# Performance work log

Hardware: AMD Instinct MI355X
Metric: run time of the kernel (lower is better)

The kernel has to match this reference:

```python
import jax, jax.numpy as jnp
import numpy as np
import math

N_HEADS = 8
INPUT_DIM = 128
EMBED_DIM = 128
KEY_DIM = 16
VAL_DIM = 16
BATCH = 2
SEQ = 4096


def setup_inputs() -> dict:
    key = jax.random.key(0)
    kq, kh, km, k1, k2, k3, k4 = jax.random.split(key, 7)
    q = jax.random.normal(kq, (BATCH, SEQ, INPUT_DIM), dtype=jnp.float32)
    h = jax.random.normal(kh, (BATCH, SEQ, INPUT_DIM), dtype=jnp.float32)
    mask = jax.random.randint(km, (BATCH, SEQ, SEQ), 0, 2).astype(jnp.bool_)
    # uniform(-stdv, stdv) with stdv = 1/sqrt(last_dim), matching init_parameters()
    def uni(k, shape):
        stdv = 1.0 / math.sqrt(shape[-1])
        return jax.random.uniform(k, shape, jnp.float32, -stdv, stdv)
    W_query = uni(k1, (N_HEADS, INPUT_DIM, KEY_DIM))
    W_key = uni(k2, (N_HEADS, INPUT_DIM, KEY_DIM))
    W_val = uni(k3, (N_HEADS, INPUT_DIM, VAL_DIM))
    W_out = uni(k4, (N_HEADS, VAL_DIM, EMBED_DIM))
    return {"q": q, "h": h, "mask": mask, "W_query": W_query,
            "W_key": W_key, "W_val": W_val, "W_out": W_out}


def reference(q, h, mask, W_query, W_key, W_val, W_out):
    norm = 1.0 / math.sqrt(KEY_DIM)
    # per-head projections: (h,b,n,k)
    Q = jnp.einsum('bni,hik->hbnk', q, W_query)
    K = jnp.einsum('bmi,hik->hbmk', h, W_key)
    V = jnp.einsum('bmi,hiv->hbmv', h, W_val)
    # full dense score tensor (h,b,n,m) — matches original materialization
    compat = norm * jnp.einsum('hbnk,hbmk->hbnm', Q, K)
    m = mask[None]  # broadcast over heads
    compat = jnp.where(m, -jnp.inf, compat)
    attn = jax.nn.softmax(compat, axis=-1)
    attn = jnp.where(m, 0.0, attn)
    heads = jnp.einsum('hbnm,hbmv->hbnv', attn, V)
    out = jnp.einsum('hbnv,hve->bne', heads, W_out)
    return out
```

## Files before the change

### kernel.cpp

```cpp
#include <hip/hip_runtime.h>
#include <stdint.h>

#define SEQ 4096
#define DIM 128
#define NHEADS 8
#define HDK 16

typedef __bf16 bf16x2 __attribute__((ext_vector_type(2)));
typedef __bf16 bf16x8 __attribute__((ext_vector_type(8)));
typedef float f32x16 __attribute__((ext_vector_type(16)));
typedef float f32x4 __attribute__((ext_vector_type(4)));
typedef unsigned uint2v __attribute__((ext_vector_type(2)));
typedef unsigned uint4v __attribute__((ext_vector_type(4)));

__device__ inline unsigned short f2bf(float x) {
  unsigned u = __builtin_bit_cast(unsigned, x);
  u = (u + 0x7FFFu + ((u >> 16) & 1u)) >> 16;
  return (unsigned short)u;
}
__device__ inline unsigned pkbf(float lo, float hi) {
  return (unsigned)f2bf(lo) | ((unsigned)f2bf(hi) << 16);
}
__device__ inline unsigned pkbf_fast(float lo, float hi) {
  bf16x2 t;
  t[0] = (__bf16)lo;
  t[1] = (__bf16)hi;
  return __builtin_bit_cast(unsigned, t);
}
__device__ inline float fexp2(float x) {
#if __has_builtin(__builtin_amdgcn_exp2f)
  return __builtin_amdgcn_exp2f(x);
#else
  return exp2f(x);
#endif
}
__device__ inline float keep_and(float e, unsigned mrsi, int kvc) {
#if __has_builtin(__builtin_amdgcn_sbfe)
  const unsigned m = (unsigned)__builtin_amdgcn_sbfe((int)mrsi, kvc, 1);
#else
  const unsigned m = (unsigned)(((int)(mrsi << (31 - kvc))) >> 31);
#endif
  return __builtin_bit_cast(float, __builtin_bit_cast(unsigned, e) & m);
}

__global__ __launch_bounds__(256) void k_pre(
    const float* __restrict__ qin, const float* __restrict__ hin,
    const float* __restrict__ Wq, const float* __restrict__ Wk,
    const float* __restrict__ Wv, const void* __restrict__ maskp,
    unsigned short* __restrict__ Qp, unsigned short* __restrict__ Kp,
    unsigned short* __restrict__ Vt32, unsigned* __restrict__ bits) {
  __shared__ float Wl[128][128];
  __shared__ float inl[8][128];
  const int bid = (int)blockIdx.x;
  const int tid = threadIdx.x;

  if (bid >= 896) {
    unsigned* Vt32w = (unsigned*)Vt32;
    const int base = (bid - 896) * 256 + tid;
    #pragma unroll
    for (int j = 0; j < 32; ++j) {
      const int w = base + j * 1024;
      const int bh = w >> 11, n2 = w & 2047;
      Vt32w[((size_t)bh * 32 + 16) * 2048 + n2] = 0x3F803F80u;
    }
    return;
  }

  if (bid >= 384) {
    unsigned (*mlds)[17] = (unsigned (*)[17])Wl;
    const unsigned*      mw = (const unsigned*)maskp;
    const unsigned char* m8 = (const unsigned char*)maskp;
    bool wordmode = true;
    #pragma unroll
    for (int i = 0; i < 32; ++i) {
      unsigned w = mw[i];
      if (!(w == 0u || w == 1u || w == 0x3F800000u)) wordmode = false;
    }
    const int mb = bid - 384;
    const int b = mb >> 8;
    const int rowbase = (mb & 255) * 16;
    const int kt = tid & 127;
    #pragma unroll
    for (int p = 0; p < 8; ++p) {
      const int rl = p * 2 + (tid >> 7);
      const size_t g = ((size_t)b * SEQ + rowbase + rl) * SEQ + kt * 32;
      unsigned word = 0;
      if (wordmode) {
        uint4v w0 = *(const uint4v*)(mw + g);
        uint4v w1 = *(const uint4v*)(mw + g + 4);
        uint4v w2 = *(const uint4v*)(mw + g + 8);
        uint4v w3 = *(const uint4v*)(mw + g + 12);
        uint4v w4 = *(const uint4v*)(mw + g + 16);
        uint4v w5 = *(const uint4v*)(mw + g + 20);
        uint4v w6 = *(const uint4v*)(mw + g + 24);
        uint4v w7 = *(const uint4v*)(mw + g + 28);
        const uint4v wv[8] = { w0, w1, w2, w3, w4, w5, w6, w7 };
        #pragma unroll
        for (int j = 0; j < 8; ++j)
          #pragma unroll
          for (int e = 0; e < 4; ++e) {
            const unsigned w = wv[j][e];
            word |= ((w | (0u - w)) >> 31) << (4 * j + e);
          }
      } else {
        uint4v c0 = *(const uint4v*)(m8 + g);
        uint4v c1 = *(const uint4v*)(m8 + g + 16);
        const uint4v cv[2] = { c0, c1 };
        #pragma unroll
        for (int j = 0; j < 2; ++j)
          #pragma unroll
          for (int e = 0; e < 4; ++e) {
            unsigned w = cv[j][e];
            #pragma unroll
            for (int by = 0; by < 4; ++by) {
              word |= ((w & 0xFFu) ? 1u : 0u) << (16 * j + 4 * e + by);
              w >>= 8;
            }
          }
      }
      mlds[kt][rl] = word;
    }
    __syncthreads();
    #pragma unroll
    for (int j = 0; j < 8; ++j) {
      const int idx = tid + 256 * j;
      const int k2 = idx >> 4, rl = idx & 15;
      bits[((size_t)b * 128 + k2) * SEQ + rowbase + rl] = mlds[k2][rl];
    }
    return;
  }

  const int mat = bid >> 7;
  const int xb  = bid & 127;
  const float* in = (mat == 0) ? qin : hin;
  const float* W  = (mat == 0) ? Wq : (mat == 1 ? Wk : Wv);
  for (int e = tid; e < 128 * 128; e += 256) {
    int i = e >> 7, c = e & 127;
    Wl[i][c] = W[((size_t)((c >> 4) * 128 + i)) * 16 + (c & 15)];
  }
  const int r  = tid >> 5;
  const int cg = (tid & 31) << 2;
  const size_t rb = (size_t)xb * 64;
  const float SCALE_Q = 0.25f * 1.4426950408889634f;
  for (int pass = 0; pass < 8; ++pass) {
    __syncthreads();
    size_t row0 = rb + pass * 8;
    for (int e = tid; e < 8 * 128; e += 256)
      inl[e >> 7][e & 127] = in[(row0 + (e >> 7)) * 128 + (e & 127)];
    __syncthreads();
    f32x4 acc = {0.f, 0.f, 0.f, 0.f};
    #pragma unroll 8
    for (int i = 0; i < 128; ++i) {
      float a = inl[r][i];
      acc += a * *(const f32x4*)&Wl[i][cg];
    }
    size_t grow = row0 + r;
    if (mat == 0) {
      uint2v o = { pkbf(acc[0] * SCALE_Q, acc[1] * SCALE_Q),
                   pkbf(acc[2] * SCALE_Q, acc[3] * SCALE_Q) };
      *(uint2v*)(Qp + grow * DIM + cg) = o;
    } else if (mat == 1) {
      uint2v o = { pkbf(acc[0], acc[1]), pkbf(acc[2], acc[3]) };
      *(uint2v*)(Kp + grow * DIM + cg) = o;
    } else {
      size_t b = grow >> 12, n = grow & 4095;
      #pragma unroll
      for (int j = 0; j < 4; ++j) {
        const int c = cg + j;
        Vt32[((size_t)(b * 8 + (c >> 4)) * 32 + (c & 15)) * SEQ + n] =
            f2bf(acc[j]);
      }
    }
  }
}

__global__ __launch_bounds__(512, 4) void k_flash(
    const unsigned short* __restrict__ Qp, const unsigned short* __restrict__ Kp,
    const unsigned short* __restrict__ Vt32, const unsigned* __restrict__ bits,
    float* __restrict__ parts, float* __restrict__ Lb, int NT) {
  const int tid  = threadIdx.x;
  const int wv   = tid >> 6;
  const int lane = tid & 63;
  const int q    = lane & 31;
  const int hi   = lane >> 5;
  const int h    = wv;
  const int sp   = blockIdx.x >> 8;
  const int bqb  = blockIdx.x & 255;
  const int b    = bqb >> 7;
  const int qb   = (bqb & 127) << 5;
  const int kt0  = sp * NT;

  const bf16x8 qfrag =
      *(const bf16x8*)(Qp + ((size_t)b * SEQ + qb + q) * DIM + h * HDK + hi * 8);
  const unsigned short* kbase =
      Kp + ((size_t)b * SEQ) * DIM + h * HDK + hi * 8 + (size_t)q * DIM;
  const int qv = q < 16 ? q : 16;
  const unsigned short* vbase =
      Vt32 + ((size_t)(b * 8 + h) * 32 + qv) * SEQ + hi * 8;
  const unsigned* bq = bits + ((size_t)b * 128 + kt0) * SEQ + qb + q;

  int koff = (kt0 << 5) * DIM;
  int boff = 0;
  int voff = kt0 << 5;

  unsigned mr0 = bq[0], mr1 = bq[SEQ];
  bf16x8 kf0 = *(const bf16x8*)(kbase + koff);
  bf16x8 kf1 = *(const bf16x8*)(kbase + koff + 32 * DIM);
  bf16x8 vf0 = *(const bf16x8*)(vbase + voff);
  bf16x8 vf1 = *(const bf16x8*)(vbase + voff + 16);
  bf16x8 vf2 = *(const bf16x8*)(vbase + voff + 32);
  bf16x8 vf3 = *(const bf16x8*)(vbase + voff + 48);

  f32x16 oacc = {};
  const int niter = NT >> 1;

  for (int t = 0; t < niter; ++t) {
    f32x16 z16 = {};
    f32x16 st0 = __builtin_amdgcn_mfma_f32_32x32x16_bf16(kf0, qfrag, z16, 0, 0, 0);
    f32x16 st1 = __builtin_amdgcn_mfma_f32_32x32x16_bf16(kf1, qfrag, z16, 0, 0, 0);

    const int adv = (t + 1 < niter) ? 1 : 0;
    const unsigned mrn0 = bq[boff + adv * 2 * SEQ];
    const unsigned mrn1 = bq[boff + adv * 2 * SEQ + SEQ];
    const bf16x8 kfn0 = *(const bf16x8*)(kbase + koff + adv * 64 * DIM);
    const bf16x8 kfn1 = *(const bf16x8*)(kbase + koff + adv * 64 * DIM + 32 * DIM);
    const int vnoff = voff + adv * 64;
    const bf16x8 vn0 = *(const bf16x8*)(vbase + vnoff);
    const bf16x8 vn1 = *(const bf16x8*)(vbase + vnoff + 16);
    const bf16x8 vn2 = *(const bf16x8*)(vbase + vnoff + 32);
    const bf16x8 vn3 = *(const bf16x8*)(vbase + vnoff + 48);

    const unsigned mrsi0 = ~(mr0 >> (hi << 2));
    const unsigned mrsi1 = ~(mr1 >> (hi << 2));

    #pragma unroll
    for (int T = 0; T < 2; ++T) {
      const unsigned mrsi = T ? mrsi1 : mrsi0;
      #pragma unroll
      for (int sl = 0; sl < 2; ++sl) {
        float pe[8];
        #pragma unroll
        for (int j = 0; j < 8; ++j) {
          const int r = sl * 8 + j;
          const int kvc = (r & 3) + 8 * (r >> 2);
          pe[j] = keep_and(fexp2(T ? st1[r] : st0[r]), mrsi, kvc);
        }
        const unsigned a0 = pkbf_fast(pe[0], pe[1]);
        const unsigned a1 = pkbf_fast(pe[2], pe[3]);
        const unsigned b0 = pkbf_fast(pe[4], pe[5]);
        const unsigned b1 = pkbf_fast(pe[6], pe[7]);
        const uint2v s0 = __builtin_amdgcn_permlane32_swap(a0, b0, false, false);
        const uint2v s1 = __builtin_amdgcn_permlane32_swap(a1, b1, false, false);
        const uint4v w = { s0.x, s1.x, s0.y, s1.y };
        const bf16x8 pfrag = __builtin_bit_cast(bf16x8, w);
        const bf16x8 vf = (T == 0) ? (sl == 0 ? vf0 : vf1)
                                   : (sl == 0 ? vf2 : vf3);
        oacc = __builtin_amdgcn_mfma_f32_32x32x16_bf16(vf, pfrag, oacc, 0, 0, 0);
      }
    }
    kf0 = kfn0; kf1 = kfn1; mr0 = mrn0; mr1 = mrn1;
    vf0 = vn0; vf1 = vn1; vf2 = vn2; vf3 = vn3;
    koff += adv * 64 * DIM;
    boff += adv * 2 * SEQ;
    voff += adv * 64;
  }

  const size_t row = (size_t)b * SEQ + qb + q;
  float* hp = parts + ((size_t)sp * 2 * SEQ + row) * DIM + h * HDK;
  f32x4 w0 = { oacc[0], oacc[1], oacc[2], oacc[3] };
  f32x4 w1 = { oacc[4], oacc[5], oacc[6], oacc[7] };
  *(f32x4*)(hp + 4 * hi)     = w0;
  *(f32x4*)(hp + 8 + 4 * hi) = w1;
  if (hi == 0)
    Lb[((size_t)sp * 2 * SEQ + row) * NHEADS + h] = oacc[8];
}

__global__ __launch_bounds__(256) void k_oproj(
    const float* __restrict__ parts, const float* __restrict__ Lb,
    const float* __restrict__ Wo, float* __restrict__ out, int NS) {
  __shared__ float Wl[128][128];
  __shared__ float inl[8][128];
  for (int e = threadIdx.x; e < 128 * 128; e += 256) Wl[e >> 7][e & 127] = Wo[e];
  const int r  = threadIdx.x >> 5;
  const int cg = (threadIdx.x & 31) << 2;
  const int h  = cg >> 4;
  const size_t R  = (size_t)2 * SEQ;
  const size_t rb = (size_t)blockIdx.x * 16;
  for (int pass = 0; pass < 2; ++pass) {
    __syncthreads();
    const size_t row = rb + pass * 8 + r;
    float l;
    f32x4 acc;
    if (NS == 4) {
      const float l0 = Lb[(0 * R + row) * NHEADS + h];
      const float l1 = Lb[(1 * R + row) * NHEADS + h];
      const float l2 = Lb[(2 * R + row) * NHEADS + h];
      const float l3 = Lb[(3 * R + row) * NHEADS + h];
      const f32x4 p0 = *(const f32x4*)&parts[(0 * R + row) * DIM + cg];
      const f32x4 p1 = *(const f32x4*)&parts[(1 * R + row) * DIM + cg];
      const f32x4 p2 = *(const f32x4*)&parts[(2 * R + row) * DIM + cg];
      const f32x4 p3 = *(const f32x4*)&parts[(3 * R + row) * DIM + cg];
      l = (l0 + l1) + (l2 + l3);
      acc = (p0 + p1) + (p2 + p3);
    } else {
      l = 0.f;
      acc = f32x4{0.f, 0.f, 0.f, 0.f};
      for (int sp = 0; sp < NS; ++sp) {
        l += Lb[(sp * R + row) * NHEADS + h];
        acc += *(const f32x4*)&parts[(sp * R + row) * DIM + cg];
      }
    }
    const float rinv = l > 0.f ? 1.0f / l : 0.f;
    *(f32x4*)&inl[r][cg] = acc * rinv;
    __syncthreads();
    f32x4 o = {0.f, 0.f, 0.f, 0.f};
    #pragma unroll 8
    for (int i = 0; i < 128; ++i) o += inl[r][i] * *(const f32x4*)&Wl[i][cg];
    *(f32x4*)(out + row * 128 + cg) = o;
  }
}

extern "C" void kernel_launch(void* const* d_in, const int* in_sizes, int n_in,
                              void* d_out, int out_size, void* d_ws, size_t ws_size,
                              hipStream_t stream) {
  const float* qin = (const float*)d_in[0];
  const float* hin = (const float*)d_in[1];
  const void* mask = d_in[2];
  const float* Wq  = (const float*)d_in[3];
  const float* Wk  = (const float*)d_in[4];
  const float* Wv  = (const float*)d_in[5];
  const float* Wo  = (const float*)d_in[6];
  float* out = (float*)d_out;
  char* ws = (char*)d_ws;

  const size_t MAT   = (size_t)2 * SEQ * DIM;
  const size_t VMAT  = (size_t)16 * 32 * SEQ;
  const size_t R     = (size_t)2 * SEQ;
  const size_t BITS  = (size_t)2 * 128 * SEQ;

  int NS = 4;
  while (NS > 1) {
    size_t need = 2 * MAT * 2 + VMAT * 2 + BITS * 4 +
                  (size_t)NS * (R * DIM * 4 + R * NHEADS * 4);
    if (need <= ws_size) break;
    NS >>= 1;
  }
  const int NT = 128 / NS;

  unsigned short* Qp    = (unsigned short*)ws;
  unsigned short* Kp    = Qp + MAT;
  unsigned short* Vt32  = Kp + MAT;
  unsigned*       bits  = (unsigned*)(Vt32 + VMAT);
  float*          parts = (float*)(bits + BITS);
  float*          Lb    = parts + (size_t)NS * R * DIM;

  k_pre<<<900, 256, 0, stream>>>(qin, hin, Wq, Wk, Wv, mask, Qp, Kp, Vt32, bits);
  k_flash<<<256 * NS, 512, 0, stream>>>(Qp, Kp, Vt32, bits, parts, Lb, NT);
  k_oproj<<<512, 256, 0, stream>>>(parts, Lb, Wo, out, NS);
}
```

Measured before the change: 130.9 us.

## Fuse mask bit-packing into flash kernel via shared memory

Mask packing moves out of the preprocessing kernel and into the flash kernel. Each block packs its own 32-query by NT-key-tile slice of the mask into an LDS bit table, and the inner loop reads mask words from there. This drops the global bits buffer round trip (write then re-read) and shrinks the preprocessing launch. In exchange it adds a prologue, an LDS footprint and a __syncthreads to the flash kernel, which may lower occupancy or delay the start of the MFMA pipeline.

```diff
diff --git a/kernel.cpp b/kernel.cpp
--- a/kernel.cpp
+++ b/kernel.cpp
@@ -46,86 +46,22 @@
 __global__ __launch_bounds__(256) void k_pre(
     const float* __restrict__ qin, const float* __restrict__ hin,
     const float* __restrict__ Wq, const float* __restrict__ Wk,
-    const float* __restrict__ Wv, const void* __restrict__ maskp,
+    const float* __restrict__ Wv,
     unsigned short* __restrict__ Qp, unsigned short* __restrict__ Kp,
-    unsigned short* __restrict__ Vt32, unsigned* __restrict__ bits) {
+    unsigned short* __restrict__ Vt32) {
   __shared__ float Wl[128][128];
   __shared__ float inl[8][128];
   const int bid = (int)blockIdx.x;
   const int tid = threadIdx.x;
 
-  if (bid >= 896) {
+  if (bid >= 384) {
     unsigned* Vt32w = (unsigned*)Vt32;
-    const int base = (bid - 896) * 256 + tid;
+    const int base = (bid - 384) * 256 + tid;
     #pragma unroll
     for (int j = 0; j < 32; ++j) {
       const int w = base + j * 1024;
       const int bh = w >> 11, n2 = w & 2047;
       Vt32w[((size_t)bh * 32 + 16) * 2048 + n2] = 0x3F803F80u;
-    }
-    return;
-  }
-
-  if (bid >= 384) {
-    unsigned (*mlds)[17] = (unsigned (*)[17])Wl;
-    const unsigned*      mw = (const unsigned*)maskp;
-    const unsigned char* m8 = (const unsigned char*)maskp;
-    bool wordmode = true;
-    #pragma unroll
-    for (int i = 0; i < 32; ++i) {
-      unsigned w = mw[i];
-      if (!(w == 0u || w == 1u || w == 0x3F800000u)) wordmode = false;
-    }
-    const int mb = bid - 384;
-    const int b = mb >> 8;
-    const int rowbase = (mb & 255) * 16;
-    const int kt = tid & 127;
-    #pragma unroll
-    for (int p = 0; p < 8; ++p) {
-      const int rl = p * 2 + (tid >> 7);
-      const size_t g = ((size_t)b * SEQ + rowbase + rl) * SEQ + kt * 32;
-      unsigned word = 0;
-      if (wordmode) {
-        uint4v w0 = *(const uint4v*)(mw + g);
-        uint4v w1 = *(const uint4v*)(mw + g + 4);
-        uint4v w2 = *(const uint4v*)(mw + g + 8);
-        uint4v w3 = *(const uint4v*)(mw + g + 12);
-        uint4v w4 = *(const uint4v*)(mw + g + 16);
-        uint4v w5 = *(const uint4v*)(mw + g + 20);
-        uint4v w6 = *(const uint4v*)(mw + g + 24);
-        uint4v w7 = *(const uint4v*)(mw + g + 28);
-        const uint4v wv[8] = { w0, w1, w2, w3, w4, w5, w6, w7 };
-        #pragma unroll
-        for (int j = 0; j < 8; ++j)
-          #pragma unroll
-          for (int e = 0; e < 4; ++e) {
-            const unsigned w = wv[j][e];
-            word |= ((w | (0u - w)) >> 31) << (4 * j + e);
-          }
-      } else {
-        uint4v c0 = *(const uint4v*)(m8 + g);
-        uint4v c1 = *(const uint4v*)(m8 + g + 16);
-        const uint4v cv[2] = { c0, c1 };
-        #pragma unroll
-        for (int j = 0; j < 2; ++j)
-          #pragma unroll
-          for (int e = 0; e < 4; ++e) {
-            unsigned w = cv[j][e];
-            #pragma unroll
-            for (int by = 0; by < 4; ++by) {
-              word |= ((w & 0xFFu) ? 1u : 0u) << (16 * j + 4 * e + by);
-              w >>= 8;
-            }
-          }
-      }
-      mlds[kt][rl] = word;
-    }
-    __syncthreads();
-    #pragma unroll
-    for (int j = 0; j < 8; ++j) {
-      const int idx = tid + 256 * j;
-      const int k2 = idx >> 4, rl = idx & 15;
-      bits[((size_t)b * 128 + k2) * SEQ + rowbase + rl] = mlds[k2][rl];
     }
     return;
   }
@@ -176,8 +112,9 @@
 
 __global__ __launch_bounds__(512, 4) void k_flash(
     const unsigned short* __restrict__ Qp, const unsigned short* __restrict__ Kp,
-    const unsigned short* __restrict__ Vt32, const unsigned* __restrict__ bits,
-    float* __restrict__ parts, float* __restrict__ Lb, int NT) {
+    const unsigned short* __restrict__ Vt32, const void* __restrict__ maskp,
+    float* __restrict__ parts, float* __restrict__ Lb, int NT, int lgNT) {
+  __shared__ unsigned lbits[32][129];
   const int tid  = threadIdx.x;
   const int wv   = tid >> 6;
   const int lane = tid & 63;
@@ -190,6 +127,49 @@
   const int qb   = (bqb & 127) << 5;
   const int kt0  = sp * NT;
 
+  {
+    const unsigned*      mw = (const unsigned*)maskp;
+    const unsigned char* m8 = (const unsigned char*)maskp;
+    bool wm = true;
+    #pragma unroll
+    for (int i = 0; i < 32; ++i) {
+      unsigned w = mw[i];
+      if (!(w == 0u || w == 1u || w == 0x3F800000u)) wm = false;
+    }
+    const int W = NT << 5;
+    for (int w = tid; w < W; w += 512) {
+      const int q_  = w >> lgNT;
+      const int kt_ = w & (NT - 1);
+      const size_t g =
+          ((size_t)b * SEQ + qb + q_) * SEQ + ((size_t)(kt0 + kt_) << 5);
+      unsigned word = 0;
+      if (wm) {
+        #pragma unroll
+        for (int c = 0; c < 8; ++c) {
+          const uint4v v = *(const uint4v*)(mw + g + 4 * c);
+          #pragma unroll
+          for (int e = 0; e < 4; ++e)
+            word |= ((v[e] | (0u - v[e])) >> 31) << (4 * c + e);
+        }
+      } else {
+        #pragma unroll
+        for (int c = 0; c < 2; ++c) {
+          const uint4v v = *(const uint4v*)(m8 + g + 16 * c);
+          #pragma unroll
+          for (int e = 0; e < 4; ++e) {
+            unsigned x = v[e];
+            #pragma unroll
+            for (int by = 0; by < 4; ++by) {
+              word |= ((x & 0xFFu) ? 1u : 0u) << (16 * c + 4 * e + by);
+              x >>= 8;
+            }
+          }
+        }
+      }
+      lbits[q_][kt_] = word;
+    }
+  }
+
   const bf16x8 qfrag =
       *(const bf16x8*)(Qp + ((size_t)b * SEQ + qb + q) * DIM + h * HDK + hi * 8);
   const unsigned short* kbase =
@@ -197,13 +177,10 @@
   const int qv = q < 16 ? q : 16;
   const unsigned short* vbase =
       Vt32 + ((size_t)(b * 8 + h) * 32 + qv) * SEQ + hi * 8;
-  const unsigned* bq = bits + ((size_t)b * 128 + kt0) * SEQ + qb + q;
 
   int koff = (kt0 << 5) * DIM;
-  int boff = 0;
   int voff = kt0 << 5;
 
-  unsigned mr0 = bq[0], mr1 = bq[SEQ];
   bf16x8 kf0 = *(const bf16x8*)(kbase + koff);
   bf16x8 kf1 = *(const bf16x8*)(kbase + koff + 32 * DIM);
   bf16x8 vf0 = *(const bf16x8*)(vbase + voff);
@@ -211,6 +188,8 @@
   bf16x8 vf2 = *(const bf16x8*)(vbase + voff + 32);
   bf16x8 vf3 = *(const bf16x8*)(vbase + voff + 48);
 
+  __syncthreads();
+
   f32x16 oacc = {};
   const int niter = NT >> 1;
 
@@ -219,9 +198,10 @@
     f32x16 st0 = __builtin_amdgcn_mfma_f32_32x32x16_bf16(kf0, qfrag, z16, 0, 0, 0);
     f32x16 st1 = __builtin_amdgcn_mfma_f32_32x32x16_bf16(kf1, qfrag, z16, 0, 0, 0);
 
+    const unsigned mr0 = lbits[q][2 * t];
+    const unsigned mr1 = lbits[q][2 * t + 1];
+
     const int adv = (t + 1 < niter) ? 1 : 0;
-    const unsigned mrn0 = bq[boff + adv * 2 * SEQ];
-    const unsigned mrn1 = bq[boff + adv * 2 * SEQ + SEQ];
     const bf16x8 kfn0 = *(const bf16x8*)(kbase + koff + adv * 64 * DIM);
     const bf16x8 kfn1 = *(const bf16x8*)(kbase + koff + adv * 64 * DIM + 32 * DIM);
     const int vnoff = voff + adv * 64;
@@ -258,10 +238,9 @@
         oacc = __builtin_amdgcn_mfma_f32_32x32x16_bf16(vf, pfrag, oacc, 0, 0, 0);
       }
     }
-    kf0 = kfn0; kf1 = kfn1; mr0 = mrn0; mr1 = mrn1;
+    kf0 = kfn0; kf1 = kfn1;
     vf0 = vn0; vf1 = vn1; vf2 = vn2; vf3 = vn3;
     koff += adv * 64 * DIM;
-    boff += adv * 2 * SEQ;
     voff += adv * 64;
   }
 
@@ -336,25 +315,25 @@
   const size_t MAT   = (size_t)2 * SEQ * DIM;
   const size_t VMAT  = (size_t)16 * 32 * SEQ;
   const size_t R     = (size_t)2 * SEQ;
-  const size_t BITS  = (size_t)2 * 128 * SEQ;
 
   int NS = 4;
   while (NS > 1) {
-    size_t need = 2 * MAT * 2 + VMAT * 2 + BITS * 4 +
+    size_t need = 2 * MAT * 2 + VMAT * 2 +
                   (size_t)NS * (R * DIM * 4 + R * NHEADS * 4);
     if (need <= ws_size) break;
     NS >>= 1;
   }
   const int NT = 128 / NS;
+  int lgNT = 0;
+  while ((1 << lgNT) < NT) ++lgNT;
 
   unsigned short* Qp    = (unsigned short*)ws;
   unsigned short* Kp    = Qp + MAT;
   unsigned short* Vt32  = Kp + MAT;
-  unsigned*       bits  = (unsigned*)(Vt32 + VMAT);
-  float*          parts = (float*)(bits + BITS);
+  float*          parts = (float*)(Vt32 + VMAT);
   float*          Lb    = parts + (size_t)NS * R * DIM;
 
-  k_pre<<<900, 256, 0, stream>>>(qin, hin, Wq, Wk, Wv, mask, Qp, Kp, Vt32, bits);
-  k_flash<<<256 * NS, 512, 0, stream>>>(Qp, Kp, Vt32, bits, parts, Lb, NT);
+  k_pre<<<388, 256, 0, stream>>>(qin, hin, Wq, Wk, Wv, Qp, Kp, Vt32);
+  k_flash<<<256 * NS, 512, 0, stream>>>(Qp, Kp, Vt32, mask, parts, Lb, NT, lgNT);
   k_oproj<<<512, 256, 0, stream>>>(parts, Lb, Wo, out, NS);
 }
```

After: 147.7 us. 12.8% more time.
